# Optimization experiments

Measured on AMD Instinct MI355X. Metric: run time of the kernel, lower is better.

Reference implementation:

```python
import jax, jax.numpy as jnp
import numpy as np

B, T, C, H = 4, 2048, 1024, 16
HS = C // H          # 64
DFF = 4 * C          # 4096
EPS = 1e-5


def _layernorm(x, g, b):
    mu = jnp.mean(x, axis=-1, keepdims=True)
    var = jnp.mean(jnp.square(x - mu), axis=-1, keepdims=True)
    return (x - mu) * jax.lax.rsqrt(var + EPS) * g + b


def setup_inputs() -> dict:
    key = jax.random.key(0)
    ks = jax.random.split(key, 12)
    s = 0.02
    return {
        "x": jax.random.normal(ks[0], (B, T, C), jnp.float32),
        "Wq": jax.random.normal(ks[1], (H, C, HS), jnp.float32) * s,
        "Wk": jax.random.normal(ks[2], (H, C, HS), jnp.float32) * s,
        "Wv": jax.random.normal(ks[3], (H, C, HS), jnp.float32) * s,
        "Wproj": jax.random.normal(ks[4], (C, C), jnp.float32) * s,
        "bproj": jnp.zeros((C,), jnp.float32),
        "ln1_g": jnp.ones((C,), jnp.float32),
        "ln1_b": jnp.zeros((C,), jnp.float32),
        "ln2_g": jnp.ones((C,), jnp.float32),
        "ln2_b": jnp.zeros((C,), jnp.float32),
        "W1": jax.random.normal(ks[5], (C, DFF), jnp.float32) * s,
        "b1": jnp.zeros((DFF,), jnp.float32),
        "W2": jax.random.normal(ks[6], (DFF, C), jnp.float32) * s,
        "b2": jnp.zeros((C,), jnp.float32),
    }


def reference(x, Wq, Wk, Wv, Wproj, bproj, ln1_g, ln1_b, ln2_g, ln2_b, W1, b1, W2, b2):
    Tn = x.shape[1]
    Cn = x.shape[2]
    # --- self-attention on ln1(x) ---
    h = _layernorm(x, ln1_g, ln1_b)
    q = jnp.einsum('btc,hcd->bhtd', h, Wq)
    k = jnp.einsum('btc,hcd->bhtd', h, Wk)
    v = jnp.einsum('btc,hcd->bhtd', h, Wv)
    # NOTE: original scales by C**-0.5 (full embed dim), not head_size**-0.5
    scores = jnp.einsum('bhtd,bhsd->bhts', q, k) * (Cn ** -0.5)
    mask = jnp.tril(jnp.ones((Tn, Tn), dtype=bool))
    scores = jnp.where(mask, scores, jnp.float32(-jnp.inf))
    att = jax.nn.softmax(scores, axis=-1)
    o = jnp.einsum('bhts,bhsd->bhtd', att, v)          # [B,H,T,HS]
    o = o.transpose(0, 2, 1, 3).reshape(x.shape)       # concat heads -> [B,T,C]
    x = x + o @ Wproj + bproj
    # --- feed-forward on ln2(x) ---
    h2 = _layernorm(x, ln2_g, ln2_b)
    x = x + jax.nn.relu(h2 @ W1 + b1) @ W2 + b2
    return x
```

## Files before the change

### kernel.cpp

```cpp
#include <hip/hip_runtime.h>
#include <hip/hip_bf16.h>
#include <stdint.h>

typedef __attribute__((ext_vector_type(8))) __bf16 bf16x8;
typedef __attribute__((ext_vector_type(4))) __bf16 bf16x4;
typedef __attribute__((ext_vector_type(4))) float f32x4;
typedef __attribute__((ext_vector_type(16))) float f32x16;
typedef __attribute__((ext_vector_type(4))) unsigned int u32x4;

typedef const __attribute__((address_space(1))) void* gas_ptr;
typedef __attribute__((address_space(3))) void* las_ptr;

static __device__ __forceinline__ void gload_lds16(const void* g, void* l) {
  __builtin_amdgcn_global_load_lds((gas_ptr)g, (las_ptr)l, 16, 0, 0);
}

static __device__ __forceinline__ unsigned int cvt_pk(float lo, float hi) {
  unsigned int r;
  asm("v_cvt_pk_bf16_f32 %0, %1, %2" : "=v"(r) : "v"(lo), "v"(hi));
  return r;
}

static __device__ __forceinline__ bf16x8 pack_frag(unsigned int a, unsigned int b,
                                                   unsigned int c, unsigned int d) {
  u32x4 t = {a, b, c, d};
  return __builtin_bit_cast(bf16x8, t);
}

static __device__ __forceinline__ void vm4() {
  asm volatile("s_waitcnt vmcnt(4)" ::: "memory");
}
static __device__ __forceinline__ void vm0() {
  asm volatile("s_waitcnt vmcnt(0)" ::: "memory");
}
static __device__ __forceinline__ void lgkm0sb() {
  asm volatile("s_waitcnt lgkmcnt(0)" ::: "memory");
  __builtin_amdgcn_sched_barrier(0);
}
static __device__ __forceinline__ void bar() {
  asm volatile("" ::: "memory");
  __builtin_amdgcn_s_barrier();
  asm volatile("" ::: "memory");
}

__global__ void transpose_cvt(const float* __restrict__ in, __bf16* __restrict__ out,
                              int R, int S) {
  __shared__ float t[32][33];
  int tx = threadIdx.x, ty = threadIdx.y;
  int r0 = blockIdx.y * 32, s0 = blockIdx.x * 32;
#pragma unroll
  for (int i = 0; i < 4; ++i) {
    int r = r0 + ty + i * 8;
    if (r < R && (s0 + tx) < S) t[ty + i * 8][tx] = in[(size_t)r * S + s0 + tx];
  }
  __syncthreads();
#pragma unroll
  for (int i = 0; i < 4; ++i) {
    int s = s0 + ty + i * 8;
    if (s < S && (r0 + tx) < R) out[(size_t)s * R + r0 + tx] = (__bf16)t[tx][ty + i * 8];
  }
}

__global__ void qkv_repack(const float* __restrict__ Wq, const float* __restrict__ Wk,
                           const float* __restrict__ Wv, __bf16* __restrict__ outT) {
  __shared__ float t[32][33];
  int z = blockIdx.z, sel = z >> 4, h = z & 15;
  const float* in = (sel == 0 ? Wq : sel == 1 ? Wk : Wv) + (size_t)h * 1024 * 64;
  __bf16* out = outT + (size_t)(sel * 1024 + h * 64) * 1024;
  int tx = threadIdx.x, ty = threadIdx.y;
  int r0 = blockIdx.y * 32, s0 = blockIdx.x * 32;
#pragma unroll
  for (int i = 0; i < 4; ++i)
    t[ty + i * 8][tx] = in[(size_t)(r0 + ty + i * 8) * 64 + s0 + tx];
  __syncthreads();
#pragma unroll
  for (int i = 0; i < 4; ++i)
    out[(size_t)(s0 + ty + i * 8) * 1024 + r0 + tx] = (__bf16)t[tx][ty + i * 8];
}

__global__ __launch_bounds__(256) void ln_kernel(const float* __restrict__ x,
                                                 const float* __restrict__ g,
                                                 const float* __restrict__ b,
                                                 __bf16* __restrict__ out) {
  __shared__ float red[8];
  int row = blockIdx.x, tid = threadIdx.x;
  float4 v = ((const float4*)(x + (size_t)row * 1024))[tid];
  float s = v.x + v.y + v.z + v.w;
  float s2 = v.x * v.x + v.y * v.y + v.z * v.z + v.w * v.w;
#pragma unroll
  for (int m = 1; m < 64; m <<= 1) { s += __shfl_xor(s, m); s2 += __shfl_xor(s2, m); }
  if ((tid & 63) == 0) { red[tid >> 6] = s; red[4 + (tid >> 6)] = s2; }
  __syncthreads();
  s = red[0] + red[1] + red[2] + red[3];
  s2 = red[4] + red[5] + red[6] + red[7];
  float mu = s * (1.0f / 1024.0f);
  float var = s2 * (1.0f / 1024.0f) - mu * mu;
  float rs = rsqrtf(var + 1e-5f);
  float4 gg = ((const float4*)g)[tid];
  float4 bb = ((const float4*)b)[tid];
  bf16x4 o4;
  o4[0] = (__bf16)((v.x - mu) * rs * gg.x + bb.x);
  o4[1] = (__bf16)((v.y - mu) * rs * gg.y + bb.y);
  o4[2] = (__bf16)((v.z - mu) * rs * gg.z + bb.z);
  o4[3] = (__bf16)((v.w - mu) * rs * gg.w + bb.w);
  *(bf16x4*)(out + (size_t)row * 1024 + tid * 4) = o4;
}

__global__ __launch_bounds__(256) void ff2_reduce(float* __restrict__ out,
                                                  const __bf16* __restrict__ p0,
                                                  const __bf16* __restrict__ p1,
                                                  const float* __restrict__ b2) {
  int i = blockIdx.x * 256 + threadIdx.x;
  float4 v = ((const float4*)out)[i];
  bf16x4 a = ((const bf16x4*)p0)[i];
  bf16x4 b = ((const bf16x4*)p1)[i];
  float4 bb = ((const float4*)b2)[i & 255];
  v.x += (float)a[0] + (float)b[0] + bb.x;
  v.y += (float)a[1] + (float)b[1] + bb.y;
  v.z += (float)a[2] + (float)b[2] + bb.z;
  v.w += (float)a[3] + (float)b[3] + bb.w;
  ((float4*)out)[i] = v;
}

template <int EPI>
__global__ __launch_bounds__(256, 3) void gemm2p(const __bf16* __restrict__ A,
                                                 const __bf16* __restrict__ Bt,
                                                 void* __restrict__ Cout,
                                                 const float* __restrict__ bias,
                                                 const float* __restrict__ resid,
                                                 __bf16* __restrict__ q_out,
                                                 __bf16* __restrict__ k_out,
                                                 __bf16* __restrict__ vt_out,
                                                 int M, int N, int K, int NBN) {
  __shared__ __align__(16) char lds[49152];
  const int tid = threadIdx.x;
  const int l = tid & 63, w = tid >> 6;
  const int lr = l & 15, lg = l >> 4;

  int nwg = gridDim.x;
  int cpx = nwg >> 3;
  int orig = blockIdx.x;
  int wgid = (orig & 7) * cpx + (orig >> 3);
  int bn = wgid % NBN, bm = wgid / NBN;
  int n0 = bn * 128, m0 = bm * 128;

  const int Kloop = K / (int)gridDim.z;
  const int NT = Kloop >> 5;
  const size_t K2 = (size_t)K * 2;
  const size_t koff = (size_t)blockIdx.z * Kloop * 2;

  const int srow = tid >> 2;
  const int sslot = ((tid & 3) ^ ((tid >> 4) & 3)) << 4;
  const char* aA = (const char*)A + (size_t)(m0 + srow) * K2 + koff + sslot;
  const char* aB = (const char*)Bt + (size_t)(n0 + srow) * K2 + koff + sslot;

  auto stage = [&](int bufi, int kt) {
    char* d = lds + bufi * 16384 + tid * 16;
    const char* sA = aA + (size_t)kt * 64;
    const char* sB = aB + (size_t)kt * 64;
    gload_lds16(sA, d);
    gload_lds16(sA + (size_t)64 * K2, d + 4096);
    gload_lds16(sB, d + 8192);
    gload_lds16(sB + (size_t)64 * K2, d + 12288);
  };

  const int arow0 = ((w >> 1) * 64 + lr) * 64;
  const int brow0 = ((w & 1) * 64 + lr) * 64;
  const int cs = ((lg ^ (lr >> 2)) & 3) << 4;

  f32x4 acc[4][4];
#pragma unroll
  for (int mi = 0; mi < 4; ++mi)
#pragma unroll
    for (int ni = 0; ni < 4; ++ni)
#pragma unroll
      for (int e = 0; e < 4; ++e) acc[mi][ni][e] = 0.0f;

  stage(0, 0);
  stage(1, NT > 1 ? 1 : 0);
  vm4();
  bar();

  for (int t = 0; t < NT; ++t) {
    if (t + 2 < NT) stage((t + 2) % 3, t + 2);
    const char* buf = lds + (t % 3) * 16384;
    bf16x8 af[4], bfr[4];
#pragma unroll
    for (int i = 0; i < 4; ++i)
      af[i] = *(const bf16x8*)(buf + arow0 + i * 1024 + cs);
#pragma unroll
    for (int i = 0; i < 4; ++i)
      bfr[i] = *(const bf16x8*)(buf + 8192 + brow0 + i * 1024 + cs);
    lgkm0sb();
    __builtin_amdgcn_s_setprio(1);
#pragma unroll
    for (int mi = 0; mi < 4; ++mi)
#pragma unroll
      for (int ni = 0; ni < 4; ++ni)
        acc[mi][ni] = __builtin_amdgcn_mfma_f32_16x16x32_bf16(af[mi], bfr[ni], acc[mi][ni], 0, 0, 0);
    __builtin_amdgcn_s_setprio(0);
    if (t + 2 < NT) vm4(); else vm0();
    bar();
  }

#pragma unroll
  for (int mi = 0; mi < 4; ++mi) {
    int rowb = m0 + (w >> 1) * 64 + mi * 16 + lg * 4;
#pragma unroll
    for (int e = 0; e < 4; ++e) {
      int row = rowb + e;
#pragma unroll
      for (int ni = 0; ni < 4; ++ni) {
        int col = n0 + (w & 1) * 64 + ni * 16 + lr;
        float v = acc[mi][ni][e];
        size_t idx = (size_t)row * N + col;
        if (EPI == 0) {
          ((__bf16*)Cout)[idx] = (__bf16)v;
        } else if (EPI == 1) {
          ((float*)Cout)[idx] = resid[idx] + v + bias[col];
        } else if (EPI == 2) {
          v += bias[col];
          ((__bf16*)Cout)[idx] = (__bf16)fmaxf(v, 0.0f);
        } else if (EPI == 5) {
          (blockIdx.z ? k_out : q_out)[idx] = (__bf16)v;
        } else {
          int b = row >> 11, t = row & 2047;
          int sel = col >> 10, cc = col & 1023, h = cc >> 6, d = cc & 63;
          int bh = b * 16 + h;
          __bf16 val = (__bf16)v;
          if (sel == 0)
            q_out[((size_t)bh * 64 + d) * 2048 + t] = val;
          else if (sel == 1)
            k_out[((size_t)bh * 2048 + t) * 64 + d] = val;
          else
            vt_out[((size_t)bh * 64 + d) * 2048 + t] = val;
        }
      }
    }
  }
}

__global__ __launch_bounds__(256) void attn_kernel3(const __bf16* __restrict__ Qt,
                                                    const __bf16* __restrict__ Kh,
                                                    const __bf16* __restrict__ Vt,
                                                    __bf16* __restrict__ o) {
  __shared__ __align__(16) char Klds[8192];
  __shared__ __align__(16) char Vlds[8192];
  int tid = threadIdx.x;
  int l = tid & 63, w = tid >> 6;
  int lq = l & 31, hi = l >> 5;
  int p = blockIdx.x, bh = blockIdx.y;
  int b = bh >> 4, h = bh & 15;

  const char* Kbase = (const char*)(Kh + (size_t)bh * 2048 * 64);
  const char* Vbase = (const char*)(Vt + (size_t)bh * 64 * 2048);
  const __bf16* Qbase = Qt + (size_t)bh * 64 * 2048;
  __bf16* Obase = o + (size_t)b * 2048 * 1024 + h * 64;

  int srow = tid >> 3;
  int schunk = (tid & 7) * 16;
  int sw0 = (srow & 7) << 4;
  char* kd0 = Klds + tid * 16;
  char* kd1 = Klds + 4096 + tid * 16;
  char* vd0 = Vlds + tid * 16;
  char* vd1 = Vlds + 4096 + tid * 16;
  int swz = (lq & 7) << 4;

  for (int sweep = 0; sweep < 2; ++sweep) {
    int t = (sweep == 0) ? p : 15 - p;
    int qw = t * 128 + w * 32;
    int qglob = qw + lq;

    bf16x8 qb[4];
    const __bf16* qsrc = Qbase + (size_t)(hi * 8) * 2048 + qw + lq;
#pragma unroll
    for (int s = 0; s < 4; ++s)
#pragma unroll
      for (int j = 0; j < 8; ++j)
        qb[s][j] = qsrc[(size_t)(s * 16 + j) * 2048];

    f32x16 oacc0, oacc1;
#pragma unroll
    for (int i = 0; i < 16; ++i) { oacc0[i] = 0.0f; oacc1[i] = 0.0f; }
    float m_q = -3.0e38f, l_q = 0.0f;

    int nkb = 2 * t + 2;
    for (int kb = 0; kb < nkb; ++kb) {
      int s0 = kb * 64;
      __syncthreads();
      gload_lds16(Kbase + (size_t)(s0 + srow) * 128 + (schunk ^ sw0), kd0);
      gload_lds16(Kbase + (size_t)(s0 + srow + 32) * 128 + (schunk ^ sw0), kd1);
      gload_lds16(Vbase + (size_t)srow * 4096 + s0 * 2 + (schunk ^ sw0), vd0);
      gload_lds16(Vbase + (size_t)(srow + 32) * 4096 + s0 * 2 + (schunk ^ sw0), vd1);
      __syncthreads();

      f32x16 st0, st1;
#pragma unroll
      for (int i = 0; i < 16; ++i) { st0[i] = 0.0f; st1[i] = 0.0f; }
#pragma unroll
      for (int s = 0; s < 4; ++s) {
        bf16x8 ka = *(const bf16x8*)(Klds + lq * 128 + ((s * 32 + hi * 16) ^ swz));
        st0 = __builtin_amdgcn_mfma_f32_32x32x16_bf16(ka, qb[s], st0, 0, 0, 0);
      }
#pragma unroll
      for (int s = 0; s < 4; ++s) {
        bf16x8 ka = *(const bf16x8*)(Klds + (32 + lq) * 128 + ((s * 32 + hi * 16) ^ swz));
        st1 = __builtin_amdgcn_mfma_f32_32x32x16_bf16(ka, qb[s], st1, 0, 0, 0);
      }
#pragma unroll
      for (int r = 0; r < 16; ++r) {
        int key0 = s0 + (r & 3) + 8 * (r >> 2) + 4 * hi;
        if (key0 > qglob) st0[r] = -1.0e38f;
        if (key0 + 32 > qglob) st1[r] = -1.0e38f;
      }
      float mx8[8];
#pragma unroll
      for (int i = 0; i < 8; ++i)
        mx8[i] = fmaxf(fmaxf(st0[i], st0[i + 8]), fmaxf(st1[i], st1[i + 8]));
      float mx = fmaxf(fmaxf(fmaxf(mx8[0], mx8[1]), fmaxf(mx8[2], mx8[3])),
                       fmaxf(fmaxf(mx8[4], mx8[5]), fmaxf(mx8[6], mx8[7])));
      {
        float u = mx, v = mx;
        asm("v_permlane32_swap_b32 %0, %1" : "+v"(u), "+v"(v));
        mx = fmaxf(u, v);
      }
      float mt_s = mx * 0.03125f;
      if (__any(mt_s > m_q + 8.0f)) {
        float mnew = fmaxf(m_q, mt_s);
        float scv = exp2f((m_q - mnew) * 1.44269504f);
        m_q = mnew;
        l_q *= scv;
#pragma unroll
        for (int r = 0; r < 16; ++r) {
          int qr = (r & 3) + 8 * (r >> 2) + 4 * hi;
          float scO = __shfl(scv, qr);
          oacc0[r] *= scO;
          oacc1[r] *= scO;
        }
      }
      float m2 = m_q * 1.44269504f;
#pragma unroll
      for (int r = 0; r < 16; ++r) {
        st0[r] = exp2f(fmaf(st0[r], 0.045084389f, -m2));
        st1[r] = exp2f(fmaf(st1[r], 0.045084389f, -m2));
      }
      float s8[8];
#pragma unroll
      for (int i = 0; i < 8; ++i)
        s8[i] = (st0[i] + st0[i + 8]) + (st1[i] + st1[i + 8]);
      float ps = ((s8[0] + s8[1]) + (s8[2] + s8[3])) +
                 ((s8[4] + s8[5]) + (s8[6] + s8[7]));
      {
        float u = ps, v = ps;
        asm("v_permlane32_swap_b32 %0, %1" : "+v"(u), "+v"(v));
        ps = u + v;
      }
      l_q += ps;

      {
        unsigned int w0 = cvt_pk(st0[0], st0[1]), w1 = cvt_pk(st0[2], st0[3]);
        unsigned int w2 = cvt_pk(st0[4], st0[5]), w3 = cvt_pk(st0[6], st0[7]);
        asm("v_permlane32_swap_b32 %0, %1" : "+v"(w0), "+v"(w2));
        asm("v_permlane32_swap_b32 %0, %1" : "+v"(w1), "+v"(w3));
        bf16x8 pa0 = pack_frag(w0, w1, w2, w3);
        unsigned int w4 = cvt_pk(st0[8], st0[9]), w5 = cvt_pk(st0[10], st0[11]);
        unsigned int w6 = cvt_pk(st0[12], st0[13]), w7 = cvt_pk(st0[14], st0[15]);
        asm("v_permlane32_swap_b32 %0, %1" : "+v"(w4), "+v"(w6));
        asm("v_permlane32_swap_b32 %0, %1" : "+v"(w5), "+v"(w7));
        bf16x8 pa1 = pack_frag(w4, w5, w6, w7);
        bf16x8 v00 = *(const bf16x8*)(Vlds + lq * 128 + ((hi * 16) ^ swz));
        bf16x8 v01 = *(const bf16x8*)(Vlds + (32 + lq) * 128 + ((hi * 16) ^ swz));
        bf16x8 v10 = *(const bf16x8*)(Vlds + lq * 128 + ((32 + hi * 16) ^ swz));
        bf16x8 v11 = *(const bf16x8*)(Vlds + (32 + lq) * 128 + ((32 + hi * 16) ^ swz));
        oacc0 = __builtin_amdgcn_mfma_f32_32x32x16_bf16(pa0, v00, oacc0, 0, 0, 0);
        oacc1 = __builtin_amdgcn_mfma_f32_32x32x16_bf16(pa0, v01, oacc1, 0, 0, 0);
        oacc0 = __builtin_amdgcn_mfma_f32_32x32x16_bf16(pa1, v10, oacc0, 0, 0, 0);
        oacc1 = __builtin_amdgcn_mfma_f32_32x32x16_bf16(pa1, v11, oacc1, 0, 0, 0);
      }
      {
        unsigned int w0 = cvt_pk(st1[0], st1[1]), w1 = cvt_pk(st1[2], st1[3]);
        unsigned int w2 = cvt_pk(st1[4], st1[5]), w3 = cvt_pk(st1[6], st1[7]);
        asm("v_permlane32_swap_b32 %0, %1" : "+v"(w0), "+v"(w2));
        asm("v_permlane32_swap_b32 %0, %1" : "+v"(w1), "+v"(w3));
        bf16x8 pa0 = pack_frag(w0, w1, w2, w3);
        unsigned int w4 = cvt_pk(st1[8], st1[9]), w5 = cvt_pk(st1[10], st1[11]);
        unsigned int w6 = cvt_pk(st1[12], st1[13]), w7 = cvt_pk(st1[14], st1[15]);
        asm("v_permlane32_swap_b32 %0, %1" : "+v"(w4), "+v"(w6));
        asm("v_permlane32_swap_b32 %0, %1" : "+v"(w5), "+v"(w7));
        bf16x8 pa1 = pack_frag(w4, w5, w6, w7);
        bf16x8 v00 = *(const bf16x8*)(Vlds + lq * 128 + ((64 + hi * 16) ^ swz));
        bf16x8 v01 = *(const bf16x8*)(Vlds + (32 + lq) * 128 + ((64 + hi * 16) ^ swz));
        bf16x8 v10 = *(const bf16x8*)(Vlds + lq * 128 + ((96 + hi * 16) ^ swz));
        bf16x8 v11 = *(const bf16x8*)(Vlds + (32 + lq) * 128 + ((96 + hi * 16) ^ swz));
        oacc0 = __builtin_amdgcn_mfma_f32_32x32x16_bf16(pa0, v00, oacc0, 0, 0, 0);
        oacc1 = __builtin_amdgcn_mfma_f32_32x32x16_bf16(pa0, v01, oacc1, 0, 0, 0);
        oacc0 = __builtin_amdgcn_mfma_f32_32x32x16_bf16(pa1, v10, oacc0, 0, 0, 0);
        oacc1 = __builtin_amdgcn_mfma_f32_32x32x16_bf16(pa1, v11, oacc1, 0, 0, 0);
      }
    }
#pragma unroll
    for (int r = 0; r < 16; ++r) {
      int qr = (r & 3) + 8 * (r >> 2) + 4 * hi;
      float linv = 1.0f / __shfl(l_q, qr);
      size_t row = qw + qr;
      Obase[row * 1024 + lq] = (__bf16)(oacc0[r] * linv);
      Obase[row * 1024 + 32 + lq] = (__bf16)(oacc1[r] * linv);
    }
  }
}

extern "C" void kernel_launch(void* const* d_in, const int* in_sizes, int n_in,
                              void* d_out, int out_size, void* d_ws, size_t ws_size,
                              hipStream_t stream) {
  const float* x     = (const float*)d_in[0];
  const float* Wq    = (const float*)d_in[1];
  const float* Wk    = (const float*)d_in[2];
  const float* Wv    = (const float*)d_in[3];
  const float* Wproj = (const float*)d_in[4];
  const float* bproj = (const float*)d_in[5];
  const float* ln1_g = (const float*)d_in[6];
  const float* ln1_b = (const float*)d_in[7];
  const float* ln2_g = (const float*)d_in[8];
  const float* ln2_b = (const float*)d_in[9];
  const float* W1    = (const float*)d_in[10];
  const float* b1    = (const float*)d_in[11];
  const float* W2    = (const float*)d_in[12];
  const float* b2    = (const float*)d_in[13];
  float* out = (float*)d_out;

  char* ws = (char*)d_ws;
  __bf16* actA   = (__bf16*)(ws + 0);
  __bf16* WqkvT  = (__bf16*)(ws + 16777216);
  __bf16* WprojT = (__bf16*)(ws + 23068672);
  __bf16* W1T    = (__bf16*)(ws + 25165824);
  __bf16* W2T    = (__bf16*)(ws + 33554432);
  __bf16* Qt     = (__bf16*)(ws + 41943040);
  __bf16* Kh     = (__bf16*)(ws + 58720256);
  __bf16* Vt     = (__bf16*)(ws + 75497472);
  __bf16* obuf   = (__bf16*)(ws + 92274688);
  __bf16* ff1    = Qt;
  __bf16* p0     = (__bf16*)(ws + 0);
  __bf16* p1     = (__bf16*)(ws + 16777216);

  dim3 t32x8(32, 8);
  qkv_repack<<<dim3(2, 32, 48), t32x8, 0, stream>>>(Wq, Wk, Wv, WqkvT);
  transpose_cvt<<<dim3(32, 32), t32x8, 0, stream>>>(Wproj, WprojT, 1024, 1024);
  transpose_cvt<<<dim3(128, 32), t32x8, 0, stream>>>(W1, W1T, 1024, 4096);
  transpose_cvt<<<dim3(32, 128), t32x8, 0, stream>>>(W2, W2T, 4096, 1024);

  ln_kernel<<<8192, 256, 0, stream>>>(x, ln1_g, ln1_b, actA);
  gemm2p<4><<<dim3(1536, 1, 1), 256, 0, stream>>>(actA, WqkvT, nullptr, nullptr, nullptr,
                                                  Qt, Kh, Vt, 8192, 3072, 1024, 24);
  attn_kernel3<<<dim3(8, 64), 256, 0, stream>>>(Qt, Kh, Vt, obuf);
  gemm2p<1><<<dim3(512, 1, 1), 256, 0, stream>>>(obuf, WprojT, out, bproj, x,
                                                 nullptr, nullptr, nullptr, 8192, 1024, 1024, 8);
  ln_kernel<<<8192, 256, 0, stream>>>(out, ln2_g, ln2_b, actA);
  gemm2p<2><<<dim3(2048, 1, 1), 256, 0, stream>>>(actA, W1T, ff1, b1, nullptr,
                                                  nullptr, nullptr, nullptr, 8192, 4096, 1024, 32);
  gemm2p<5><<<dim3(512, 1, 2), 256, 0, stream>>>(ff1, W2T, nullptr, nullptr, nullptr,
                                                 p0, p1, nullptr, 8192, 1024, 4096, 8);
  ff2_reduce<<<8192, 256, 0, stream>>>(out, p0, p1, b2);
}
```

Baseline: 436.0 us.

## Add 256x256 GEMM kernel and double-buffer attention K/V with causal block skip

Adds a 512-thread GEMM with 256x256 output tiles and double-buffered LDS staging, used for the QKV, FF1 and split-K FF2 matmuls. The larger tile raises operand reuse and halves global traffic per output. The attention kernel now double-buffers K/V tiles so the next block's loads overlap compute, applies the causal mask only on diagonal blocks, and skips key blocks fully above a wave's queries. The trade-offs are fewer workgroups (384 or 256 for some GEMMs, which may underfill the GPU), higher register pressure from 32 accumulators per lane, and an unswizzled LDS layout in gemm256 that may cause bank conflicts.

```diff
diff --git a/kernel.cpp b/kernel.cpp
--- a/kernel.cpp
+++ b/kernel.cpp
@@ -123,14 +123,125 @@
 }
 
 template <int EPI>
+__global__ __launch_bounds__(512) void gemm256(const __bf16* __restrict__ A,
+                                               const __bf16* __restrict__ Bt,
+                                               void* __restrict__ Cout,
+                                               const float* __restrict__ bias,
+                                               const float* __restrict__ resid,
+                                               __bf16* __restrict__ q_out,
+                                               __bf16* __restrict__ k_out,
+                                               __bf16* __restrict__ vt_out,
+                                               int M, int N, int K, int NBN) {
+  __shared__ __align__(16) char lds[65536];
+  const int tid = threadIdx.x;
+  const int l = tid & 63, w = tid >> 6;
+  const int wm = w >> 2, wn = w & 3;
+  const int lr = l & 15, lg = l >> 4;
+
+  int nwg = gridDim.x;
+  int cpx = nwg >> 3;
+  int orig = blockIdx.x;
+  int wgid = (orig & 7) * cpx + (orig >> 3);
+  int bn = wgid % NBN, bm = wgid / NBN;
+  int n0 = bn * 256, m0 = bm * 256;
+
+  const int Kloop = K / (int)gridDim.z;
+  const int NT = Kloop >> 5;
+  const size_t K2 = (size_t)K * 2;
+  const size_t koff = (size_t)blockIdx.z * Kloop * 2;
+
+  const int srow = tid >> 2;
+  const int sslot = (tid & 3) * 16;
+  const char* aA = (const char*)A + (size_t)(m0 + srow) * K2 + koff + sslot;
+  const char* aB = (const char*)Bt + (size_t)(n0 + srow) * K2 + koff + sslot;
+
+  auto stage = [&](int bufi, int kt) {
+    char* d = lds + bufi * 32768 + tid * 16;
+    const char* sA = aA + (size_t)kt * 64;
+    const char* sB = aB + (size_t)kt * 64;
+    gload_lds16(sA, d);
+    gload_lds16(sA + (size_t)128 * K2, d + 8192);
+    gload_lds16(sB, d + 16384);
+    gload_lds16(sB + (size_t)128 * K2, d + 24576);
+  };
+
+  const int arow0 = (wm * 128 + lr) * 64 + lg * 16;
+  const int brow0 = 16384 + (wn * 64 + lr) * 64 + lg * 16;
+
+  f32x4 acc[8][4];
+#pragma unroll
+  for (int mi = 0; mi < 8; ++mi)
+#pragma unroll
+    for (int ni = 0; ni < 4; ++ni)
+#pragma unroll
+      for (int e = 0; e < 4; ++e) acc[mi][ni][e] = 0.0f;
+
+  stage(0, 0);
+
+  for (int t = 0; t < NT; ++t) {
+    if (t + 1 < NT) { stage((t + 1) & 1, t + 1); vm4(); }
+    else vm0();
+    bar();
+    const char* buf = lds + (t & 1) * 32768;
+    bf16x8 af[8], bfr[4];
+#pragma unroll
+    for (int i = 0; i < 8; ++i)
+      af[i] = *(const bf16x8*)(buf + arow0 + i * 1024);
+#pragma unroll
+    for (int j = 0; j < 4; ++j)
+      bfr[j] = *(const bf16x8*)(buf + brow0 + j * 1024);
+    lgkm0sb();
+    __builtin_amdgcn_s_setprio(1);
+#pragma unroll
+    for (int mi = 0; mi < 8; ++mi)
+#pragma unroll
+      for (int ni = 0; ni < 4; ++ni)
+        acc[mi][ni] = __builtin_amdgcn_mfma_f32_16x16x32_bf16(af[mi], bfr[ni], acc[mi][ni], 0, 0, 0);
+    __builtin_amdgcn_s_setprio(0);
+    bar();
+  }
+
+#pragma unroll
+  for (int mi = 0; mi < 8; ++mi) {
+    int rowb = m0 + wm * 128 + mi * 16 + lg * 4;
+#pragma unroll
+    for (int e = 0; e < 4; ++e) {
+      int row = rowb + e;
+#pragma unroll
+      for (int ni = 0; ni < 4; ++ni) {
+        int col = n0 + wn * 64 + ni * 16 + lr;
+        float v = acc[mi][ni][e];
+        size_t idx = (size_t)row * N + col;
+        if (EPI == 0) {
+          ((__bf16*)Cout)[idx] = (__bf16)v;
+        } else if (EPI == 2) {
+          v += bias[col];
+          ((__bf16*)Cout)[idx] = (__bf16)fmaxf(v, 0.0f);
+        } else if (EPI == 5) {
+          (blockIdx.z ? k_out : q_out)[idx] = (__bf16)v;
+        } else {
+          int b = row >> 11, t2 = row & 2047;
+          int sel = col >> 10, cc = col & 1023, h = cc >> 6, d = cc & 63;
+          int bh = b * 16 + h;
+          __bf16 val = (__bf16)v;
+          if (sel == 0)
+            q_out[((size_t)bh * 64 + d) * 2048 + t2] = val;
+          else if (sel == 1)
+            k_out[((size_t)bh * 2048 + t2) * 64 + d] = val;
+          else
+            vt_out[((size_t)bh * 64 + d) * 2048 + t2] = val;
+        }
+      }
+    }
+  }
+}
+
+template <int EPI>
 __global__ __launch_bounds__(256, 3) void gemm2p(const __bf16* __restrict__ A,
                                                  const __bf16* __restrict__ Bt,
                                                  void* __restrict__ Cout,
                                                  const float* __restrict__ bias,
                                                  const float* __restrict__ resid,
-                                                 __bf16* __restrict__ q_out,
-                                                 __bf16* __restrict__ k_out,
-                                                 __bf16* __restrict__ vt_out,
                                                  int M, int N, int K, int NBN) {
   __shared__ __align__(16) char lds[49152];
   const int tid = threadIdx.x;
@@ -144,15 +255,13 @@
   int bn = wgid % NBN, bm = wgid / NBN;
   int n0 = bn * 128, m0 = bm * 128;
 
-  const int Kloop = K / (int)gridDim.z;
-  const int NT = Kloop >> 5;
+  const int NT = K >> 5;
   const size_t K2 = (size_t)K * 2;
-  const size_t koff = (size_t)blockIdx.z * Kloop * 2;
 
   const int srow = tid >> 2;
   const int sslot = ((tid & 3) ^ ((tid >> 4) & 3)) << 4;
-  const char* aA = (const char*)A + (size_t)(m0 + srow) * K2 + koff + sslot;
-  const char* aB = (const char*)Bt + (size_t)(n0 + srow) * K2 + koff + sslot;
+  const char* aA = (const char*)A + (size_t)(m0 + srow) * K2 + sslot;
+  const char* aB = (const char*)Bt + (size_t)(n0 + srow) * K2 + sslot;
 
   auto stage = [&](int bufi, int kt) {
     char* d = lds + bufi * 16384 + tid * 16;
@@ -214,38 +323,22 @@
         int col = n0 + (w & 1) * 64 + ni * 16 + lr;
         float v = acc[mi][ni][e];
         size_t idx = (size_t)row * N + col;
-        if (EPI == 0) {
+        if (EPI == 1) {
+          ((float*)Cout)[idx] = resid[idx] + v + bias[col];
+        } else {
           ((__bf16*)Cout)[idx] = (__bf16)v;
-        } else if (EPI == 1) {
-          ((float*)Cout)[idx] = resid[idx] + v + bias[col];
-        } else if (EPI == 2) {
-          v += bias[col];
-          ((__bf16*)Cout)[idx] = (__bf16)fmaxf(v, 0.0f);
-        } else if (EPI == 5) {
-          (blockIdx.z ? k_out : q_out)[idx] = (__bf16)v;
-        } else {
-          int b = row >> 11, t = row & 2047;
-          int sel = col >> 10, cc = col & 1023, h = cc >> 6, d = cc & 63;
-          int bh = b * 16 + h;
-          __bf16 val = (__bf16)v;
-          if (sel == 0)
-            q_out[((size_t)bh * 64 + d) * 2048 + t] = val;
-          else if (sel == 1)
-            k_out[((size_t)bh * 2048 + t) * 64 + d] = val;
-          else
-            vt_out[((size_t)bh * 64 + d) * 2048 + t] = val;
         }
       }
     }
   }
 }
 
-__global__ __launch_bounds__(256) void attn_kernel3(const __bf16* __restrict__ Qt,
+__global__ __launch_bounds__(256) void attn_kernel4(const __bf16* __restrict__ Qt,
                                                     const __bf16* __restrict__ Kh,
                                                     const __bf16* __restrict__ Vt,
                                                     __bf16* __restrict__ o) {
-  __shared__ __align__(16) char Klds[8192];
-  __shared__ __align__(16) char Vlds[8192];
+  __shared__ __align__(16) char Klds[16384];
+  __shared__ __align__(16) char Vlds[16384];
   int tid = threadIdx.x;
   int l = tid & 63, w = tid >> 6;
   int lq = l & 31, hi = l >> 5;
@@ -260,11 +353,16 @@
   int srow = tid >> 3;
   int schunk = (tid & 7) * 16;
   int sw0 = (srow & 7) << 4;
-  char* kd0 = Klds + tid * 16;
-  char* kd1 = Klds + 4096 + tid * 16;
-  char* vd0 = Vlds + tid * 16;
-  char* vd1 = Vlds + 4096 + tid * 16;
   int swz = (lq & 7) << 4;
+
+  auto stageKV = [&](int bufi, int s0) {
+    char* kd = Klds + bufi * 8192 + tid * 16;
+    char* vd = Vlds + bufi * 8192 + tid * 16;
+    gload_lds16(Kbase + (size_t)(s0 + srow) * 128 + (schunk ^ sw0), kd);
+    gload_lds16(Kbase + (size_t)(s0 + srow + 32) * 128 + (schunk ^ sw0), kd + 4096);
+    gload_lds16(Vbase + (size_t)srow * 4096 + s0 * 2 + (schunk ^ sw0), vd);
+    gload_lds16(Vbase + (size_t)(srow + 32) * 4096 + s0 * 2 + (schunk ^ sw0), vd + 4096);
+  };
 
   for (int sweep = 0; sweep < 2; ++sweep) {
     int t = (sweep == 0) ? p : 15 - p;
@@ -285,118 +383,123 @@
     float m_q = -3.0e38f, l_q = 0.0f;
 
     int nkb = 2 * t + 2;
+    stageKV(0, 0);
     for (int kb = 0; kb < nkb; ++kb) {
       int s0 = kb * 64;
-      __syncthreads();
-      gload_lds16(Kbase + (size_t)(s0 + srow) * 128 + (schunk ^ sw0), kd0);
-      gload_lds16(Kbase + (size_t)(s0 + srow + 32) * 128 + (schunk ^ sw0), kd1);
-      gload_lds16(Vbase + (size_t)srow * 4096 + s0 * 2 + (schunk ^ sw0), vd0);
-      gload_lds16(Vbase + (size_t)(srow + 32) * 4096 + s0 * 2 + (schunk ^ sw0), vd1);
-      __syncthreads();
-
-      f32x16 st0, st1;
-#pragma unroll
-      for (int i = 0; i < 16; ++i) { st0[i] = 0.0f; st1[i] = 0.0f; }
-#pragma unroll
-      for (int s = 0; s < 4; ++s) {
-        bf16x8 ka = *(const bf16x8*)(Klds + lq * 128 + ((s * 32 + hi * 16) ^ swz));
-        st0 = __builtin_amdgcn_mfma_f32_32x32x16_bf16(ka, qb[s], st0, 0, 0, 0);
+      if (kb + 1 < nkb) { stageKV((kb + 1) & 1, s0 + 64); vm4(); }
+      else vm0();
+      bar();
+      const char* Kb = Klds + (kb & 1) * 8192;
+      const char* Vb = Vlds + (kb & 1) * 8192;
+
+      if (s0 <= qw + 31) {
+        f32x16 st0, st1;
+#pragma unroll
+        for (int i = 0; i < 16; ++i) { st0[i] = 0.0f; st1[i] = 0.0f; }
+#pragma unroll
+        for (int s = 0; s < 4; ++s) {
+          bf16x8 ka = *(const bf16x8*)(Kb + lq * 128 + ((s * 32 + hi * 16) ^ swz));
+          st0 = __builtin_amdgcn_mfma_f32_32x32x16_bf16(ka, qb[s], st0, 0, 0, 0);
+        }
+#pragma unroll
+        for (int s = 0; s < 4; ++s) {
+          bf16x8 ka = *(const bf16x8*)(Kb + (32 + lq) * 128 + ((s * 32 + hi * 16) ^ swz));
+          st1 = __builtin_amdgcn_mfma_f32_32x32x16_bf16(ka, qb[s], st1, 0, 0, 0);
+        }
+        if (s0 + 63 > qw) {
+#pragma unroll
+          for (int r = 0; r < 16; ++r) {
+            int key0 = s0 + (r & 3) + 8 * (r >> 2) + 4 * hi;
+            if (key0 > qglob) st0[r] = -1.0e38f;
+            if (key0 + 32 > qglob) st1[r] = -1.0e38f;
+          }
+        }
+        float mx8[8];
+#pragma unroll
+        for (int i = 0; i < 8; ++i)
+          mx8[i] = fmaxf(fmaxf(st0[i], st0[i + 8]), fmaxf(st1[i], st1[i + 8]));
+        float mx = fmaxf(fmaxf(fmaxf(mx8[0], mx8[1]), fmaxf(mx8[2], mx8[3])),
+                         fmaxf(fmaxf(mx8[4], mx8[5]), fmaxf(mx8[6], mx8[7])));
+        {
+          float u = mx, v = mx;
+          asm("v_permlane32_swap_b32 %0, %1" : "+v"(u), "+v"(v));
+          mx = fmaxf(u, v);
+        }
+        float mt_s = mx * 0.03125f;
+        if (__any(mt_s > m_q + 8.0f)) {
+          float mnew = fmaxf(m_q, mt_s);
+          float scv = exp2f((m_q - mnew) * 1.44269504f);
+          m_q = mnew;
+          l_q *= scv;
+#pragma unroll
+          for (int r = 0; r < 16; ++r) {
+            int qr = (r & 3) + 8 * (r >> 2) + 4 * hi;
+            float scO = __shfl(scv, qr);
+            oacc0[r] *= scO;
+            oacc1[r] *= scO;
+          }
+        }
+        float m2 = m_q * 1.44269504f;
+#pragma unroll
+        for (int r = 0; r < 16; ++r) {
+          st0[r] = exp2f(fmaf(st0[r], 0.045084389f, -m2));
+          st1[r] = exp2f(fmaf(st1[r], 0.045084389f, -m2));
+        }
+        float s8[8];
+#pragma unroll
+        for (int i = 0; i < 8; ++i)
+          s8[i] = (st0[i] + st0[i + 8]) + (st1[i] + st1[i + 8]);
+        float ps = ((s8[0] + s8[1]) + (s8[2] + s8[3])) +
+                   ((s8[4] + s8[5]) + (s8[6] + s8[7]));
+        {
+          float u = ps, v = ps;
+          asm("v_permlane32_swap_b32 %0, %1" : "+v"(u), "+v"(v));
+          ps = u + v;
+        }
+        l_q += ps;
+
+        {
+          unsigned int w0 = cvt_pk(st0[0], st0[1]), w1 = cvt_pk(st0[2], st0[3]);
+          unsigned int w2 = cvt_pk(st0[4], st0[5]), w3 = cvt_pk(st0[6], st0[7]);
+          asm("v_permlane32_swap_b32 %0, %1" : "+v"(w0), "+v"(w2));
+          asm("v_permlane32_swap_b32 %0, %1" : "+v"(w1), "+v"(w3));
+          bf16x8 pa0 = pack_frag(w0, w1, w2, w3);
+          unsigned int w4 = cvt_pk(st0[8], st0[9]), w5 = cvt_pk(st0[10], st0[11]);
+          unsigned int w6 = cvt_pk(st0[12], st0[13]), w7 = cvt_pk(st0[14], st0[15]);
+          asm("v_permlane32_swap_b32 %0, %1" : "+v"(w4), "+v"(w6));
+          asm("v_permlane32_swap_b32 %0, %1" : "+v"(w5), "+v"(w7));
+          bf16x8 pa1 = pack_frag(w4, w5, w6, w7);
+          bf16x8 v00 = *(const bf16x8*)(Vb + lq * 128 + ((hi * 16) ^ swz));
+          bf16x8 v01 = *(const bf16x8*)(Vb + (32 + lq) * 128 + ((hi * 16) ^ swz));
+          bf16x8 v10 = *(const bf16x8*)(Vb + lq * 128 + ((32 + hi * 16) ^ swz));
+          bf16x8 v11 = *(const bf16x8*)(Vb + (32 + lq) * 128 + ((32 + hi * 16) ^ swz));
+          oacc0 = __builtin_amdgcn_mfma_f32_32x32x16_bf16(pa0, v00, oacc0, 0, 0, 0);
+          oacc1 = __builtin_amdgcn_mfma_f32_32x32x16_bf16(pa0, v01, oacc1, 0, 0, 0);
+          oacc0 = __builtin_amdgcn_mfma_f32_32x32x16_bf16(pa1, v10, oacc0, 0, 0, 0);
+          oacc1 = __builtin_amdgcn_mfma_f32_32x32x16_bf16(pa1, v11, oacc1, 0, 0, 0);
+        }
+        {
+          unsigned int w0 = cvt_pk(st1[0], st1[1]), w1 = cvt_pk(st1[2], st1[3]);
+          unsigned int w2 = cvt_pk(st1[4], st1[5]), w3 = cvt_pk(st1[6], st1[7]);
+          asm("v_permlane32_swap_b32 %0, %1" : "+v"(w0), "+v"(w2));
+          asm("v_permlane32_swap_b32 %0, %1" : "+v"(w1), "+v"(w3));
+          bf16x8 pa0 = pack_frag(w0, w1, w2, w3);
+          unsigned int w4 = cvt_pk(st1[8], st1[9]), w5 = cvt_pk(st1[10], st1[11]);
+          unsigned int w6 = cvt_pk(st1[12], st1[13]), w7 = cvt_pk(st1[14], st1[15]);
+          asm("v_permlane32_swap_b32 %0, %1" : "+v"(w4), "+v"(w6));
+          asm("v_permlane32_swap_b32 %0, %1" : "+v"(w5), "+v"(w7));
+          bf16x8 pa1 = pack_frag(w4, w5, w6, w7);
+          bf16x8 v00 = *(const bf16x8*)(Vb + lq * 128 + ((64 + hi * 16) ^ swz));
+          bf16x8 v01 = *(const bf16x8*)(Vb + (32 + lq) * 128 + ((64 + hi * 16) ^ swz));
+          bf16x8 v10 = *(const bf16x8*)(Vb + lq * 128 + ((96 + hi * 16) ^ swz));
+          bf16x8 v11 = *(const bf16x8*)(Vb + (32 + lq) * 128 + ((96 + hi * 16) ^ swz));
+          oacc0 = __builtin_amdgcn_mfma_f32_32x32x16_bf16(pa0, v00, oacc0, 0, 0, 0);
+          oacc1 = __builtin_amdgcn_mfma_f32_32x32x16_bf16(pa0, v01, oacc1, 0, 0, 0);
+          oacc0 = __builtin_amdgcn_mfma_f32_32x32x16_bf16(pa1, v10, oacc0, 0, 0, 0);
+          oacc1 = __builtin_amdgcn_mfma_f32_32x32x16_bf16(pa1, v11, oacc1, 0, 0, 0);
+        }
       }
-#pragma unroll
-      for (int s = 0; s < 4; ++s) {
-        bf16x8 ka = *(const bf16x8*)(Klds + (32 + lq) * 128 + ((s * 32 + hi * 16) ^ swz));
-        st1 = __builtin_amdgcn_mfma_f32_32x32x16_bf16(ka, qb[s], st1, 0, 0, 0);
-      }
-#pragma unroll
-      for (int r = 0; r < 16; ++r) {
-        int key0 = s0 + (r & 3) + 8 * (r >> 2) + 4 * hi;
-        if (key0 > qglob) st0[r] = -1.0e38f;
-        if (key0 + 32 > qglob) st1[r] = -1.0e38f;
-      }
-      float mx8[8];
-#pragma unroll
-      for (int i = 0; i < 8; ++i)
-        mx8[i] = fmaxf(fmaxf(st0[i], st0[i + 8]), fmaxf(st1[i], st1[i + 8]));
-      float mx = fmaxf(fmaxf(fmaxf(mx8[0], mx8[1]), fmaxf(mx8[2], mx8[3])),
-                       fmaxf(fmaxf(mx8[4], mx8[5]), fmaxf(mx8[6], mx8[7])));
-      {
-        float u = mx, v = mx;
-        asm("v_permlane32_swap_b32 %0, %1" : "+v"(u), "+v"(v));
-        mx = fmaxf(u, v);
-      }
-      float mt_s = mx * 0.03125f;
-      if (__any(mt_s > m_q + 8.0f)) {
-        float mnew = fmaxf(m_q, mt_s);
-        float scv = exp2f((m_q - mnew) * 1.44269504f);
-        m_q = mnew;
-        l_q *= scv;
-#pragma unroll
-        for (int r = 0; r < 16; ++r) {
-          int qr = (r & 3) + 8 * (r >> 2) + 4 * hi;
-          float scO = __shfl(scv, qr);
-          oacc0[r] *= scO;
-          oacc1[r] *= scO;
-        }
-      }
-      float m2 = m_q * 1.44269504f;
-#pragma unroll
-      for (int r = 0; r < 16; ++r) {
-        st0[r] = exp2f(fmaf(st0[r], 0.045084389f, -m2));
-        st1[r] = exp2f(fmaf(st1[r], 0.045084389f, -m2));
-      }
-      float s8[8];
-#pragma unroll
-      for (int i = 0; i < 8; ++i)
-        s8[i] = (st0[i] + st0[i + 8]) + (st1[i] + st1[i + 8]);
-      float ps = ((s8[0] + s8[1]) + (s8[2] + s8[3])) +
-                 ((s8[4] + s8[5]) + (s8[6] + s8[7]));
-      {
-        float u = ps, v = ps;
-        asm("v_permlane32_swap_b32 %0, %1" : "+v"(u), "+v"(v));
-        ps = u + v;
-      }
-      l_q += ps;
-
-      {
-        unsigned int w0 = cvt_pk(st0[0], st0[1]), w1 = cvt_pk(st0[2], st0[3]);
-        unsigned int w2 = cvt_pk(st0[4], st0[5]), w3 = cvt_pk(st0[6], st0[7]);
-        asm("v_permlane32_swap_b32 %0, %1" : "+v"(w0), "+v"(w2));
-        asm("v_permlane32_swap_b32 %0, %1" : "+v"(w1), "+v"(w3));
-        bf16x8 pa0 = pack_frag(w0, w1, w2, w3);
-        unsigned int w4 = cvt_pk(st0[8], st0[9]), w5 = cvt_pk(st0[10], st0[11]);
-        unsigned int w6 = cvt_pk(st0[12], st0[13]), w7 = cvt_pk(st0[14], st0[15]);
-        asm("v_permlane32_swap_b32 %0, %1" : "+v"(w4), "+v"(w6));
-        asm("v_permlane32_swap_b32 %0, %1" : "+v"(w5), "+v"(w7));
-        bf16x8 pa1 = pack_frag(w4, w5, w6, w7);
-        bf16x8 v00 = *(const bf16x8*)(Vlds + lq * 128 + ((hi * 16) ^ swz));
-        bf16x8 v01 = *(const bf16x8*)(Vlds + (32 + lq) * 128 + ((hi * 16) ^ swz));
-        bf16x8 v10 = *(const bf16x8*)(Vlds + lq * 128 + ((32 + hi * 16) ^ swz));
-        bf16x8 v11 = *(const bf16x8*)(Vlds + (32 + lq) * 128 + ((32 + hi * 16) ^ swz));
-        oacc0 = __builtin_amdgcn_mfma_f32_32x32x16_bf16(pa0, v00, oacc0, 0, 0, 0);
-        oacc1 = __builtin_amdgcn_mfma_f32_32x32x16_bf16(pa0, v01, oacc1, 0, 0, 0);
-        oacc0 = __builtin_amdgcn_mfma_f32_32x32x16_bf16(pa1, v10, oacc0, 0, 0, 0);
-        oacc1 = __builtin_amdgcn_mfma_f32_32x32x16_bf16(pa1, v11, oacc1, 0, 0, 0);
-      }
-      {
-        unsigned int w0 = cvt_pk(st1[0], st1[1]), w1 = cvt_pk(st1[2], st1[3]);
-        unsigned int w2 = cvt_pk(st1[4], st1[5]), w3 = cvt_pk(st1[6], st1[7]);
-        asm("v_permlane32_swap_b32 %0, %1" : "+v"(w0), "+v"(w2));
-        asm("v_permlane32_swap_b32 %0, %1" : "+v"(w1), "+v"(w3));
-        bf16x8 pa0 = pack_frag(w0, w1, w2, w3);
-        unsigned int w4 = cvt_pk(st1[8], st1[9]), w5 = cvt_pk(st1[10], st1[11]);
-        unsigned int w6 = cvt_pk(st1[12], st1[13]), w7 = cvt_pk(st1[14], st1[15]);
-        asm("v_permlane32_swap_b32 %0, %1" : "+v"(w4), "+v"(w6));
-        asm("v_permlane32_swap_b32 %0, %1" : "+v"(w5), "+v"(w7));
-        bf16x8 pa1 = pack_frag(w4, w5, w6, w7);
-        bf16x8 v00 = *(const bf16x8*)(Vlds + lq * 128 + ((64 + hi * 16) ^ swz));
-        bf16x8 v01 = *(const bf16x8*)(Vlds + (32 + lq) * 128 + ((64 + hi * 16) ^ swz));
-        bf16x8 v10 = *(const bf16x8*)(Vlds + lq * 128 + ((96 + hi * 16) ^ swz));
-        bf16x8 v11 = *(const bf16x8*)(Vlds + (32 + lq) * 128 + ((96 + hi * 16) ^ swz));
-        oacc0 = __builtin_amdgcn_mfma_f32_32x32x16_bf16(pa0, v00, oacc0, 0, 0, 0);
-        oacc1 = __builtin_amdgcn_mfma_f32_32x32x16_bf16(pa0, v01, oacc1, 0, 0, 0);
-        oacc0 = __builtin_amdgcn_mfma_f32_32x32x16_bf16(pa1, v10, oacc0, 0, 0, 0);
-        oacc1 = __builtin_amdgcn_mfma_f32_32x32x16_bf16(pa1, v11, oacc1, 0, 0, 0);
-      }
+      bar();
     }
 #pragma unroll
     for (int r = 0; r < 16; ++r) {
@@ -449,15 +552,15 @@
   transpose_cvt<<<dim3(32, 128), t32x8, 0, stream>>>(W2, W2T, 4096, 1024);
 
   ln_kernel<<<8192, 256, 0, stream>>>(x, ln1_g, ln1_b, actA);
-  gemm2p<4><<<dim3(1536, 1, 1), 256, 0, stream>>>(actA, WqkvT, nullptr, nullptr, nullptr,
-                                                  Qt, Kh, Vt, 8192, 3072, 1024, 24);
-  attn_kernel3<<<dim3(8, 64), 256, 0, stream>>>(Qt, Kh, Vt, obuf);
+  gemm256<4><<<dim3(384, 1, 1), 512, 0, stream>>>(actA, WqkvT, nullptr, nullptr, nullptr,
+                                                  Qt, Kh, Vt, 8192, 3072, 1024, 12);
+  attn_kernel4<<<dim3(8, 64), 256, 0, stream>>>(Qt, Kh, Vt, obuf);
   gemm2p<1><<<dim3(512, 1, 1), 256, 0, stream>>>(obuf, WprojT, out, bproj, x,
-                                                 nullptr, nullptr, nullptr, 8192, 1024, 1024, 8);
+                                                 8192, 1024, 1024, 8);
   ln_kernel<<<8192, 256, 0, stream>>>(out, ln2_g, ln2_b, actA);
-  gemm2p<2><<<dim3(2048, 1, 1), 256, 0, stream>>>(actA, W1T, ff1, b1, nullptr,
-                                                  nullptr, nullptr, nullptr, 8192, 4096, 1024, 32);
-  gemm2p<5><<<dim3(512, 1, 2), 256, 0, stream>>>(ff1, W2T, nullptr, nullptr, nullptr,
-                                                 p0, p1, nullptr, 8192, 1024, 4096, 8);
+  gemm256<2><<<dim3(512, 1, 1), 512, 0, stream>>>(actA, W1T, ff1, b1, nullptr,
+                                                  nullptr, nullptr, nullptr, 8192, 4096, 1024, 16);
+  gemm256<5><<<dim3(128, 1, 2), 512, 0, stream>>>(ff1, W2T, nullptr, nullptr, nullptr,
+                                                  p0, p1, nullptr, 8192, 1024, 4096, 4);
   ff2_reduce<<<8192, 256, 0, stream>>>(out, p0, p1, b2);
 }
```

After: 431.0 us. No clear change (-1.2%).
